# Kernel optimization log

Hardware: AMD Instinct MI355X
Metric: run time of the kernel (lower is better)

The kernel has to match this reference:

```python
import jax, jax.numpy as jnp
import numpy as np

WT, WH, WW = 2, 8, 8
N_WIN = WT * WH * WW  # 128 tokens per window
DIM, HEADS = 192, 6
HEAD_DIM = DIM // HEADS
SCALE = HEAD_DIM ** -0.5


def _relative_position_index():
    ct, ch, cw = np.arange(WT), np.arange(WH), np.arange(WW)
    coords = np.stack(np.meshgrid(ct, ch, cw, indexing='ij'))  # (3,WT,WH,WW)
    cf = coords.reshape(3, -1)
    rel = cf[:, :, None] - cf[:, None, :]  # (3,N,N)
    rel = rel.transpose(1, 2, 0).copy()
    rel[:, :, 0] += WT - 1
    rel[:, :, 1] += WH - 1
    rel[:, :, 2] += WW - 1
    rel[:, :, 0] *= (2 * WH - 1) * (2 * WW - 1)
    rel[:, :, 1] *= 2 * WW - 1
    return rel.sum(-1)  # (N,N) int

_REL_IDX = jnp.asarray(_relative_position_index())


def _layernorm(x, g, b, eps=1e-5):
    mu = x.mean(-1, keepdims=True)
    var = ((x - mu) ** 2).mean(-1, keepdims=True)
    return (x - mu) * jax.lax.rsqrt(var + eps) * g + b


def setup_inputs() -> dict:
    key = jax.random.key(0)
    ks = jax.random.split(key, 16)
    B, T, H, W, C = 2, 8, 128, 128, DIM
    hid = 4 * C
    n_bias = (2 * WT - 1) * (2 * WH - 1) * (2 * WW - 1)
    s = lambda fan: 1.0 / np.sqrt(fan)
    return {
        'x': jax.random.normal(ks[0], (B, T, H, W, C), jnp.float32),
        'norm1_g': jnp.ones((C,), jnp.float32),
        'norm1_b': jnp.zeros((C,), jnp.float32),
        'qkv_w': jax.random.normal(ks[1], (3 * C, C), jnp.float32) * s(C),
        'qkv_b': jnp.zeros((3 * C,), jnp.float32),
        'bias_table': jax.random.normal(ks[2], (n_bias, HEADS), jnp.float32) * 0.02,
        'proj_w': jax.random.normal(ks[3], (C, C), jnp.float32) * s(C),
        'proj_b': jnp.zeros((C,), jnp.float32),
        'norm2_g': jnp.ones((C,), jnp.float32),
        'norm2_b': jnp.zeros((C,), jnp.float32),
        'fc1_w': jax.random.normal(ks[4], (hid, C), jnp.float32) * s(C),
        'fc1_b': jnp.zeros((hid,), jnp.float32),
        'fc2_w': jax.random.normal(ks[5], (C, hid), jnp.float32) * s(hid),
        'fc2_b': jnp.zeros((C,), jnp.float32),
    }


def reference(x, norm1_g, norm1_b, qkv_w, qkv_b, bias_table, proj_w, proj_b,
              norm2_g, norm2_b, fc1_w, fc1_b, fc2_w, fc2_b):
    B, T, H, W, C = x.shape
    shortcut = x
    xn = _layernorm(x, norm1_g, norm1_b)

    # window partition: (B,T,H,W,C) -> (B_, N, C)
    xw = xn.reshape(B, T // WT, WT, H // WH, WH, W // WW, WW, C)
    xw = xw.transpose(0, 1, 3, 5, 2, 4, 6, 7).reshape(-1, N_WIN, C)

    # qkv projection (torch Linear: y = x @ W.T + b)
    qkv = xw @ qkv_w.T + qkv_b  # (B_, N, 3C)
    B_ = qkv.shape[0]
    qkv = qkv.reshape(B_, N_WIN, 3, HEADS, HEAD_DIM)
    q, k, v = qkv[:, :, 0], qkv[:, :, 1], qkv[:, :, 2]  # (B_, N, h, d)

    attn = jnp.einsum('bnhd,bmhd->bhnm', q * SCALE, k)
    bias = bias_table[_REL_IDX.reshape(-1)].reshape(N_WIN, N_WIN, HEADS)
    attn = attn + bias.transpose(2, 0, 1)[None]  # (B_, h, N, N)
    attn = jax.nn.softmax(attn, axis=-1)

    out = jnp.einsum('bhnm,bmhd->bnhd', attn, v).reshape(B_, N_WIN, C)
    out = out @ proj_w.T + proj_b

    # window reverse
    out = out.reshape(B, T // WT, H // WH, W // WW, WT, WH, WW, C)
    out = out.transpose(0, 1, 4, 2, 5, 3, 6, 7).reshape(B, T, H, W, C)

    x = shortcut + out
    # MLP with residual (GELU exact, matching nn.GELU default)
    h1 = _layernorm(x, norm2_g, norm2_b) @ fc1_w.T + fc1_b
    h1 = jax.nn.gelu(h1, approximate=False)
    x = x + (h1 @ fc2_w.T + fc2_b)
    return x
```

## Files before the change

### kernel.cpp

```cpp
#include <hip/hip_runtime.h>
#include <hip/hip_bf16.h>
#include <math.h>

typedef __hip_bfloat16 bf16;
typedef __attribute__((ext_vector_type(8))) __bf16 bf16x8;
typedef __attribute__((ext_vector_type(4))) float floatx4;

#define CDIM 192
#define N_WINDOWS 2048
#define ATT_SCALE 0.17677669529663687f

__device__ inline float toF(float v) { return v; }
__device__ inline float toF(bf16 v) { return __bfloat162float(v); }

__device__ inline void gld16(const void* g, void* l) {
    __builtin_amdgcn_global_load_lds((const __attribute__((address_space(1))) uint32_t*)g,
                                     (__attribute__((address_space(3))) uint32_t*)l,
                                     16, 0, 0);
}

__device__ inline long nat_index(int wi, int n, int col) {
    int wb = wi & 15, hb = (wi >> 4) & 15, tb = (wi >> 8) & 3, bb = wi >> 10;
    int t  = tb * 2 + (n >> 6);
    int hh = hb * 8 + ((n >> 3) & 7);
    int w  = wb * 8 + (n & 7);
    return ((((long)(bb * 8 + t)) * 128 + hh) * 128 + w) * CDIM + col;
}

__launch_bounds__(256)
__global__ void cvt_w_kernel(const float* __restrict__ src, bf16* __restrict__ dst, int n) {
    int i = (blockIdx.x * 256 + threadIdx.x) * 8;
    if (i < n) {
        float4 a = *(const float4*)(src + i);
        float4 b = *(const float4*)(src + i + 4);
        bf16x8 o;
        o[0] = (__bf16)a.x; o[1] = (__bf16)a.y; o[2] = (__bf16)a.z; o[3] = (__bf16)a.w;
        o[4] = (__bf16)b.x; o[5] = (__bf16)b.y; o[6] = (__bf16)b.z; o[7] = (__bf16)b.w;
        *(bf16x8*)(dst + i) = o;
    }
}

__device__ inline float rel_bias(const float* bt, int h, int n, int m) {
    int tn = n >> 6, hn = (n >> 3) & 7, wn = n & 7;
    int tm = m >> 6, hm = (m >> 3) & 7, wm = m & 7;
    int idx = (tn - tm + 1) * 225 + (hn - hm + 7) * 15 + (wn - wm + 7);
    return bt[idx * 6 + h];
}

__launch_bounds__(256)
__global__ void bias_expand_kernel(const float* __restrict__ bt, float* __restrict__ bias6) {
    int i = blockIdx.x * 256 + threadIdx.x;
    int n = i >> 7, m = i & 127;
    #pragma unroll
    for (int h = 0; h < 6; ++h)
        bias6[h * 16384 + i] = rel_bias(bt, h, n, m);
}

template<bool WINDOWED, typename T>
__launch_bounds__(256)
__global__ void ln_kernel(const T* __restrict__ x, const float* __restrict__ g,
                          const float* __restrict__ bta, bf16* __restrict__ out,
                          int wi_base) {
    int row = blockIdx.x * 4 + (threadIdx.x >> 6);
    int lane = threadIdx.x & 63;
    long src;
    if (WINDOWED) {
        src = nat_index(wi_base + (row >> 7), row & 127, 0);
    } else {
        src = (long)row * CDIM;
    }
    float v0 = toF(x[src + lane]);
    float v1 = toF(x[src + lane + 64]);
    float v2 = toF(x[src + lane + 128]);
    float s = v0 + v1 + v2;
    float sq = v0 * v0 + v1 * v1 + v2 * v2;
    #pragma unroll
    for (int o = 32; o > 0; o >>= 1) { s += __shfl_xor(s, o); sq += __shfl_xor(sq, o); }
    float mean = s * (1.0f / 192.0f);
    float var  = sq * (1.0f / 192.0f) - mean * mean;
    float rstd = rsqrtf(fmaxf(var, 0.0f) + 1e-5f);
    long dst = (long)row * CDIM;
    out[dst + lane]       = __float2bfloat16((v0 - mean) * rstd * g[lane]       + bta[lane]);
    out[dst + lane + 64]  = __float2bfloat16((v1 - mean) * rstd * g[lane + 64]  + bta[lane + 64]);
    out[dst + lane + 128] = __float2bfloat16((v2 - mean) * rstd * g[lane + 128] + bta[lane + 128]);
}

template<typename Epi>
__launch_bounds__(256, 2)
__global__ void gemm_bt(const bf16* __restrict__ A, const bf16* __restrict__ Wt,
                        int K, int nb, Epi epi) {
    __shared__ __align__(16) bf16 sA[128 * 192];
    __shared__ __align__(16) bf16 sW[64 * 192];
    const int tid = threadIdx.x;
    const int lane = tid & 63;
    const int wv = tid >> 6;
    int gid = blockIdx.x;
    int swz = (gid & 7) * (gridDim.x >> 3) + (gid >> 3);
    const int m0 = (swz / nb) * 128;
    const int n0 = (swz % nb) * 64;

    const int colb = lane & 15, quad = lane >> 4;
    floatx4 acc[2][4] = {};

    for (int k0 = 0; k0 < K; k0 += 192) {
        if (k0) __syncthreads();
        #pragma unroll
        for (int i = 0; i < 12; ++i) {
            int t = i * 256 + tid;
            int r = t / 24, cb = (t - r * 24) * 16;
            int scb = cb ^ ((r & 7) << 4);
            gld16((const char*)(A + (long)(m0 + r) * K + k0) + scb,
                  (char*)sA + i * 4096 + wv * 1024);
        }
        #pragma unroll
        for (int i = 0; i < 6; ++i) {
            int t = i * 256 + tid;
            int r = t / 24, cb = (t - r * 24) * 16;
            int scb = cb ^ ((r & 7) << 4);
            gld16((const char*)(Wt + (long)(n0 + r) * K + k0) + scb,
                  (char*)sW + i * 4096 + wv * 1024);
        }
        __syncthreads();
        #pragma unroll
        for (int kk = 0; kk < 6; ++kk) {
            bf16x8 aF[2], bF[4];
            int cb = kk * 64 + quad * 16;
            #pragma unroll
            for (int rt = 0; rt < 2; ++rt) {
                int rr = wv * 32 + rt * 16 + colb;
                aF[rt] = *(const bf16x8*)((char*)sA + rr * 384 + (cb ^ ((rr & 7) << 4)));
            }
            #pragma unroll
            for (int ct = 0; ct < 4; ++ct) {
                int rr = ct * 16 + colb;
                bF[ct] = *(const bf16x8*)((char*)sW + rr * 384 + (cb ^ ((rr & 7) << 4)));
            }
            #pragma unroll
            for (int rt = 0; rt < 2; ++rt)
                #pragma unroll
                for (int ct = 0; ct < 4; ++ct)
                    acc[rt][ct] = __builtin_amdgcn_mfma_f32_16x16x32_bf16(aF[rt], bF[ct], acc[rt][ct], 0, 0, 0);
        }
    }
    #pragma unroll
    for (int rt = 0; rt < 2; ++rt)
        #pragma unroll
        for (int r = 0; r < 4; ++r) {
            int row = m0 + wv * 32 + rt * 16 + quad * 4 + r;
            #pragma unroll
            for (int ct = 0; ct < 4; ++ct)
                epi(row, n0 + ct * 16 + colb, acc[rt][ct][r]);
        }
}

struct EpiQKV {
    const float* bias; bf16 *q, *k, *v;
    __device__ void operator()(int row, int col, float val) const {
        val += bias[col];
        int wi = row >> 7, n = row & 127;
        int part = col / 192, rem = col - part * 192;
        int h = rem >> 5, d = rem & 31;
        long base = (long)(wi * 6 + h);
        if (part == 0)      q[(base * 128 + n) * 32 + d] = __float2bfloat16(val * ATT_SCALE);
        else if (part == 1) k[(base * 128 + n) * 32 + d] = __float2bfloat16(val);
        else                v[(base * 32 + d) * 128 + n] = __float2bfloat16(val);
    }
};

struct EpiProj {
    const float* bias; const float* x; bf16* x2; int wi_base;
    __device__ void operator()(int row, int col, float val) const {
        val += bias[col];
        long nat = nat_index(wi_base + (row >> 7), row & 127, col);
        x2[(long)row * CDIM + col] = __float2bfloat16(val + x[nat]);
    }
};

struct EpiGelu {
    const float* bias; bf16* h1;
    __device__ void operator()(int row, int col, float val) const {
        val += bias[col];
        float g = 0.5f * val * (1.0f + erff(val * 0.70710678118654752f));
        h1[(long)row * 768 + col] = __float2bfloat16(g);
    }
};

struct EpiOut {
    const float* bias; const bf16* x2; float* out; int wi_base;
    __device__ void operator()(int row, int col, float val) const {
        val += bias[col];
        long nat = nat_index(wi_base + (row >> 7), row & 127, col);
        out[nat] = val + __bfloat162float(x2[(long)row * CDIM + col]);
    }
};

__launch_bounds__(256)
__global__ void attn_kernel(const bf16* __restrict__ q, const bf16* __restrict__ k,
                            const bf16* __restrict__ vT, const float* __restrict__ bias6,
                            bf16* __restrict__ out) {
    __shared__ __align__(16) bf16 sQ[128 * 32];
    __shared__ __align__(16) bf16 sK[128 * 32];
    __shared__ __align__(16) bf16 sVT[32 * 128];
    __shared__ __align__(16) bf16 sP[128 * 128];
    const int blk = blockIdx.x;
    const int h = blk % 6;
    const int wi = blk / 6;
    const int tid = threadIdx.x, lane = tid & 63, wv = tid >> 6;
    const bf16* qg = q + (long)blk * 4096;
    const bf16* kg = k + (long)blk * 4096;
    const bf16* vg = vT + (long)blk * 4096;
    #pragma unroll
    for (int i = 0; i < 2; ++i) {
        int t = tid + i * 256;
        int r = t >> 2, cb = (t & 3) << 4;
        int d = r * 64 + (cb ^ ((r & 6) << 3));
        *(uint4*)((char*)sQ + d) = *(const uint4*)(qg + t * 8);
        *(uint4*)((char*)sK + d) = *(const uint4*)(kg + t * 8);
        int rv = t >> 4, cv = (t & 15) << 4;
        int dv = rv * 256 + (cv ^ ((rv & 7) << 4));
        *(uint4*)((char*)sVT + dv) = *(const uint4*)(vg + t * 8);
    }
    __syncthreads();

    const int mrow = wv * 32;
    const int colb = lane & 15, quad = lane >> 4;
    floatx4 zero = {0.f, 0.f, 0.f, 0.f};
    floatx4 s[2][8];
    bf16x8 aF[2];
    #pragma unroll
    for (int rt = 0; rt < 2; ++rt) {
        int rr = mrow + rt * 16 + colb;
        aF[rt] = *(const bf16x8*)((char*)sQ + rr * 64 + ((quad * 16) ^ ((rr & 6) << 3)));
    }
    #pragma unroll
    for (int ct = 0; ct < 8; ++ct) {
        int rr = ct * 16 + colb;
        bf16x8 bF = *(const bf16x8*)((char*)sK + rr * 64 + ((quad * 16) ^ ((rr & 6) << 3)));
        #pragma unroll
        for (int rt = 0; rt < 2; ++rt)
            s[rt][ct] = __builtin_amdgcn_mfma_f32_16x16x32_bf16(aF[rt], bF, zero, 0, 0, 0);
    }
    const float* bh = bias6 + h * 16384;
    #pragma unroll
    for (int rt = 0; rt < 2; ++rt) {
        #pragma unroll
        for (int r = 0; r < 4; ++r) {
            int n = mrow + rt * 16 + quad * 4 + r;
            float vals[8];
            float mx = -1e30f;
            #pragma unroll
            for (int ct = 0; ct < 8; ++ct) {
                float v = s[rt][ct][r] + bh[n * 128 + ct * 16 + colb];
                vals[ct] = v; mx = fmaxf(mx, v);
            }
            #pragma unroll
            for (int o = 1; o < 16; o <<= 1) mx = fmaxf(mx, __shfl_xor(mx, o));
            float sum = 0.f;
            #pragma unroll
            for (int ct = 0; ct < 8; ++ct) { vals[ct] = __expf(vals[ct] - mx); sum += vals[ct]; }
            #pragma unroll
            for (int o = 1; o < 16; o <<= 1) sum += __shfl_xor(sum, o);
            float inv = 1.0f / sum;
            #pragma unroll
            for (int ct = 0; ct < 8; ++ct) {
                int cwb = (ct * 16 + colb) * 2;
                *(bf16*)((char*)sP + n * 256 + (cwb ^ ((n & 7) << 4))) =
                    __float2bfloat16(vals[ct] * inv);
            }
        }
    }
    __syncthreads();
    floatx4 o[2][2] = {};
    #pragma unroll
    for (int kk = 0; kk < 4; ++kk) {
        int cbb = kk * 64 + quad * 16;
        bf16x8 aP[2];
        #pragma unroll
        for (int rt = 0; rt < 2; ++rt) {
            int rr = mrow + rt * 16 + colb;
            aP[rt] = *(const bf16x8*)((char*)sP + rr * 256 + (cbb ^ ((rr & 7) << 4)));
        }
        #pragma unroll
        for (int ct = 0; ct < 2; ++ct) {
            int rr = ct * 16 + colb;
            bf16x8 bV = *(const bf16x8*)((char*)sVT + rr * 256 + (cbb ^ ((rr & 7) << 4)));
            #pragma unroll
            for (int rt = 0; rt < 2; ++rt)
                o[rt][ct] = __builtin_amdgcn_mfma_f32_16x16x32_bf16(aP[rt], bV, o[rt][ct], 0, 0, 0);
        }
    }
    #pragma unroll
    for (int rt = 0; rt < 2; ++rt)
        #pragma unroll
        for (int ct = 0; ct < 2; ++ct)
            #pragma unroll
            for (int r = 0; r < 4; ++r) {
                int n = mrow + rt * 16 + quad * 4 + r;
                out[((long)(wi * 128 + n)) * CDIM + h * 32 + ct * 16 + colb] =
                    __float2bfloat16(o[rt][ct][r]);
            }
}

extern "C" void kernel_launch(void* const* d_in, const int* in_sizes, int n_in,
                              void* d_out, int out_size, void* d_ws, size_t ws_size,
                              hipStream_t stream) {
    const float* x      = (const float*)d_in[0];
    const float* n1g    = (const float*)d_in[1];
    const float* n1b    = (const float*)d_in[2];
    const float* qkv_w  = (const float*)d_in[3];
    const float* qkv_b  = (const float*)d_in[4];
    const float* btab   = (const float*)d_in[5];
    const float* proj_w = (const float*)d_in[6];
    const float* proj_b = (const float*)d_in[7];
    const float* n2g    = (const float*)d_in[8];
    const float* n2b    = (const float*)d_in[9];
    const float* fc1_w  = (const float*)d_in[10];
    const float* fc1_b  = (const float*)d_in[11];
    const float* fc2_w  = (const float*)d_in[12];
    const float* fc2_b  = (const float*)d_in[13];
    float* outp = (float*)d_out;

    char* ws = (char*)d_ws;

    const int NQKV = 576 * 192, NPROJ = 192 * 192, NFC1 = 768 * 192, NFC2 = 192 * 768;
    bf16* qkvW = (bf16*)ws;
    bf16* projW = qkvW + NQKV;
    bf16* fc1W = projW + NPROJ;
    bf16* fc2W = fc1W + NFC1;
    const size_t WBYTES = (size_t)(NQKV + NPROJ + NFC1 + NFC2) * 2;
    float* bias6 = (float*)(ws + WBYTES);
    const size_t BBYTES = 6UL * 128 * 128 * 4;

    cvt_w_kernel<<<NQKV / 2048, 256, 0, stream>>>(qkv_w, qkvW, NQKV);
    cvt_w_kernel<<<NPROJ / 2048, 256, 0, stream>>>(proj_w, projW, NPROJ);
    cvt_w_kernel<<<NFC1 / 2048, 256, 0, stream>>>(fc1_w, fc1W, NFC1);
    cvt_w_kernel<<<NFC2 / 2048, 256, 0, stream>>>(fc2_w, fc2W, NFC2);
    bias_expand_kernel<<<64, 256, 0, stream>>>(btab, bias6);

    const size_t per_win = 6UL * 128 * 192 * 2;
    size_t avail = ws_size > WBYTES + BBYTES ? ws_size - WBYTES - BBYTES : 0;
    int S = 512;
    while (S > 64 && (size_t)S * per_win > avail) S >>= 1;

    char* slots = ws + WBYTES + BBYTES;
    const size_t SLOT = (size_t)S * 128 * CDIM * 2;
    bf16* bufA = (bf16*)(slots);
    bf16* qb   = (bf16*)(slots + SLOT);
    bf16* kb   = (bf16*)(slots + 2 * SLOT);
    bf16* vb   = (bf16*)(slots + 3 * SLOT);
    bf16* x2   = qb;
    bf16* h1   = kb;

    for (int s0 = 0; s0 < N_WINDOWS; s0 += S) {
        ln_kernel<true, float><<<S * 32, 256, 0, stream>>>(x, n1g, n1b, bufA, s0);
        gemm_bt<EpiQKV><<<S * 9, 256, 0, stream>>>(bufA, qkvW, 192, 9, EpiQKV{qkv_b, qb, kb, vb});
        attn_kernel<<<S * 6, 256, 0, stream>>>(qb, kb, vb, bias6, bufA);
        gemm_bt<EpiProj><<<S * 3, 256, 0, stream>>>(bufA, projW, 192, 3, EpiProj{proj_b, x, x2, s0});
        ln_kernel<false, bf16><<<S * 32, 256, 0, stream>>>(x2, n2g, n2b, bufA, 0);
        gemm_bt<EpiGelu><<<S * 12, 256, 0, stream>>>(bufA, fc1W, 192, 12, EpiGelu{fc1_b, h1});
        gemm_bt<EpiOut><<<S * 3, 256, 0, stream>>>(h1, fc2W, 768, 3, EpiOut{fc2_b, x2, outp, s0});
    }
}
```

Measured before the change: 1.755 ms.

## Double-buffer GEMM K-tiles of 64 and raise occupancy to 3 blocks

The bf16 MFMA GEMM used to stage a whole 192-wide K slice of A and W into shared memory, then compute, with no overlap between loads and math. It now uses 64-wide K tiles in two ping-pong LDS buffers: the next tile's global_load_lds is issued before the MFMAs on the current tile, with one barrier per tile. LDS per block drops from 72 KB to 48 KB and launch bounds rise to 3 blocks per CU, so more blocks can hide latency. The cost is more barriers and loop iterations per K, and possibly tighter register limits under the higher occupancy bound.

```diff
diff --git a/kernel.cpp b/kernel.cpp
--- a/kernel.cpp
+++ b/kernel.cpp
@@ -86,11 +86,11 @@
 }
 
 template<typename Epi>
-__launch_bounds__(256, 2)
+__launch_bounds__(256, 3)
 __global__ void gemm_bt(const bf16* __restrict__ A, const bf16* __restrict__ Wt,
                         int K, int nb, Epi epi) {
-    __shared__ __align__(16) bf16 sA[128 * 192];
-    __shared__ __align__(16) bf16 sW[64 * 192];
+    __shared__ __align__(16) bf16 sA[2][128 * 64];
+    __shared__ __align__(16) bf16 sW[2][64 * 64];
     const int tid = threadIdx.x;
     const int lane = tid & 63;
     const int wv = tid >> 6;
@@ -98,42 +98,49 @@
     int swz = (gid & 7) * (gridDim.x >> 3) + (gid >> 3);
     const int m0 = (swz / nb) * 128;
     const int n0 = (swz % nb) * 64;
-
     const int colb = lane & 15, quad = lane >> 4;
+
     floatx4 acc[2][4] = {};
-
-    for (int k0 = 0; k0 < K; k0 += 192) {
-        if (k0) __syncthreads();
-        #pragma unroll
-        for (int i = 0; i < 12; ++i) {
-            int t = i * 256 + tid;
-            int r = t / 24, cb = (t - r * 24) * 16;
-            int scb = cb ^ ((r & 7) << 4);
-            gld16((const char*)(A + (long)(m0 + r) * K + k0) + scb,
-                  (char*)sA + i * 4096 + wv * 1024);
-        }
-        #pragma unroll
-        for (int i = 0; i < 6; ++i) {
-            int t = i * 256 + tid;
-            int r = t / 24, cb = (t - r * 24) * 16;
-            int scb = cb ^ ((r & 7) << 4);
-            gld16((const char*)(Wt + (long)(n0 + r) * K + k0) + scb,
-                  (char*)sW + i * 4096 + wv * 1024);
-        }
-        __syncthreads();
-        #pragma unroll
-        for (int kk = 0; kk < 6; ++kk) {
+    const int nt = K >> 6;
+
+    #define STAGE(b, k0)                                                        \
+        {                                                                       \
+            _Pragma("unroll")                                                   \
+            for (int i = 0; i < 4; ++i) {                                       \
+                int c = i * 256 + tid;                                          \
+                int r = c >> 3, cc = (c & 7) << 4;                              \
+                int scb = cc ^ ((r & 7) << 4);                                  \
+                gld16((const char*)(A + (long)(m0 + r) * K + (k0)) + scb,       \
+                      (char*)sA[b] + i * 4096 + wv * 1024);                     \
+            }                                                                   \
+            _Pragma("unroll")                                                   \
+            for (int i = 0; i < 2; ++i) {                                       \
+                int c = i * 256 + tid;                                          \
+                int r = c >> 3, cc = (c & 7) << 4;                              \
+                int scb = cc ^ ((r & 7) << 4);                                  \
+                gld16((const char*)(Wt + (long)(n0 + r) * K + (k0)) + scb,      \
+                      (char*)sW[b] + i * 4096 + wv * 1024);                     \
+            }                                                                   \
+        }
+
+    STAGE(0, 0);
+    __syncthreads();
+    for (int t = 0; t < nt; ++t) {
+        int cur = t & 1;
+        if (t + 1 < nt) STAGE(cur ^ 1, (t + 1) << 6);
+        #pragma unroll
+        for (int kk = 0; kk < 2; ++kk) {
             bf16x8 aF[2], bF[4];
             int cb = kk * 64 + quad * 16;
             #pragma unroll
             for (int rt = 0; rt < 2; ++rt) {
                 int rr = wv * 32 + rt * 16 + colb;
-                aF[rt] = *(const bf16x8*)((char*)sA + rr * 384 + (cb ^ ((rr & 7) << 4)));
+                aF[rt] = *(const bf16x8*)((char*)sA[cur] + rr * 128 + (cb ^ ((rr & 7) << 4)));
             }
             #pragma unroll
             for (int ct = 0; ct < 4; ++ct) {
                 int rr = ct * 16 + colb;
-                bF[ct] = *(const bf16x8*)((char*)sW + rr * 384 + (cb ^ ((rr & 7) << 4)));
+                bF[ct] = *(const bf16x8*)((char*)sW[cur] + rr * 128 + (cb ^ ((rr & 7) << 4)));
             }
             #pragma unroll
             for (int rt = 0; rt < 2; ++rt)
@@ -141,7 +148,10 @@
                 for (int ct = 0; ct < 4; ++ct)
                     acc[rt][ct] = __builtin_amdgcn_mfma_f32_16x16x32_bf16(aF[rt], bF[ct], acc[rt][ct], 0, 0, 0);
         }
-    }
+        if (t + 1 < nt) __syncthreads();
+    }
+    #undef STAGE
+
     #pragma unroll
     for (int rt = 0; rt < 2; ++rt)
         #pragma unroll
```

New measurement: 1.491 ms. -15.1%, faster.
